# Kernel tuning notes

Hardware: AMD Instinct MI355X
Metric: run time of the kernel (lower is better)

Reference implementation:

```python
import jax, jax.numpy as jnp
import numpy as np
from jax import lax

HID = 256   # hidden_size
NN = 25     # n_nodes
T = 50      # seq_len
FIN = 16    # obs_length + 4
AS = 8      # action_space
HEADS = 5   # gat_head_num
E = 100     # edges per graph
B = 256     # batch


def setup_inputs() -> dict:
    key = jax.random.key(0)
    ks = jax.random.split(key, 32)
    s = 0.02
    def p(i, shape):
        return jax.random.normal(ks[i], shape, jnp.float32) * s
    return {
        "obs": jax.random.normal(ks[0], (B, NN, T, FIN), jnp.float32),
        "obs_map": jax.random.normal(ks[1], (B, 3, 84, 84), jnp.float32),
        "edges": jax.random.randint(ks[2], (B, 2, E), 0, NN),
        "edges_feature": jax.random.normal(ks[3], (B, E, 4), jnp.float32),
        "mlp_w": p(4, (FIN, HID)), "mlp_b": p(5, (HID,)),
        "c1_w": p(6, (32, 3, 8, 8)), "c1_b": p(7, (32,)),
        "c2_w": p(8, (64, 32, 4, 4)), "c2_b": p(9, (64,)),
        "c3_w": p(10, (64, 64, 3, 3)), "c3_b": p(11, (64,)),
        "fc_w": p(12, (3136, HID)), "fc_b": p(13, (HID,)),
        "gru_wih": p(14, (3 * HID, HID)), "gru_whh": p(15, (3 * HID, HID)),
        "gru_bih": p(16, (3 * HID,)), "gru_bhh": p(17, (3 * HID,)),
        "gat_wl": p(18, (HID, HEADS * HID)), "gat_bl": p(19, (HEADS * HID,)),
        "gat_wr": p(20, (HID, HEADS * HID)), "gat_br": p(21, (HEADS * HID,)),
        "gat_att": p(22, (HEADS, HID)), "gat_bias": p(23, (HID,)),
        "hid_w": p(24, (HID, HID)), "hid_b": p(25, (HID,)),
        "out_w": p(26, (HID, 1)), "out_b": p(27, (1,)),
        "adv_w": p(28, (HID, AS)), "adv_b": p(29, (AS,)),
    }


def _cnn(x, c1w, c1b, c2w, c2b, c3w, c3b, fcw, fcb):
    # Nature-CNN encoder: [B,3,84,84] -> [B,HID]
    dn = ('NCHW', 'OIHW', 'NCHW')
    h = jax.nn.relu(lax.conv_general_dilated(x, c1w, (4, 4), 'VALID', dimension_numbers=dn) + c1b[None, :, None, None])
    h = jax.nn.relu(lax.conv_general_dilated(h, c2w, (2, 2), 'VALID', dimension_numbers=dn) + c2b[None, :, None, None])
    h = jax.nn.relu(lax.conv_general_dilated(h, c3w, (1, 1), 'VALID', dimension_numbers=dn) + c3b[None, :, None, None])
    h = h.reshape(h.shape[0], -1)  # [B, 64*7*7]
    return jax.nn.relu(h @ fcw + fcb)


def _gru_last(x, wih, whh, bih, bhh):
    # torch nn.GRU (batch_first), return final hidden state [B,H]
    H = whh.shape[1]
    xg = x @ wih.T + bih  # precompute input gates [B,T,3H]
    def step(h, xg_t):
        hg = h @ whh.T + bhh
        xr, xz, xn = jnp.split(xg_t, 3, axis=-1)
        hr, hz, hn = jnp.split(hg, 3, axis=-1)
        r = jax.nn.sigmoid(xr + hr)
        z = jax.nn.sigmoid(xz + hz)
        n = jnp.tanh(xn + r * hn)
        return (1.0 - z) * n + z * h, None
    h0 = jnp.zeros((x.shape[0], H), x.dtype)
    hT, _ = lax.scan(step, h0, jnp.swapaxes(xg, 0, 1))
    return hT


def _gat(x, ei, wl, bl, wr, br, att, gbias):
    # GATv2Conv (concat=False): one graph, x [N,H], ei [2,E'] incl. self loops
    n = x.shape[0]
    heads, ch = att.shape
    src, dst = ei[0], ei[1]
    gl = (x @ wl + bl).reshape(n, heads, ch)
    gr = (x @ wr + br).reshape(n, heads, ch)
    e = jax.nn.leaky_relu(gl[src] + gr[dst], 0.2)          # [E',H,C]
    score = jnp.einsum('ehc,hc->eh', e, att)               # [E',H]
    m = jax.ops.segment_max(score, dst, num_segments=n)
    ex = jnp.exp(score - m[dst])
    den = jax.ops.segment_sum(ex, dst, num_segments=n)
    alpha = ex / den[dst]                                   # softmax per dst node
    out = jax.ops.segment_sum(alpha[:, :, None] * gl[src], dst, num_segments=n)
    return out.mean(axis=1) + gbias, alpha                  # mean over heads (concat=False)


def reference(obs, obs_map, edges, edges_feature, mlp_w, mlp_b, c1_w, c1_b, c2_w, c2_b, c3_w, c3_b, fc_w, fc_b, gru_wih, gru_whh, gru_bih, gru_bhh, gat_wl, gat_bl, gat_wr, gat_br, gat_att, gat_bias, hid_w, hid_b, out_w, out_b, adv_w, adv_b):
    bsz, n = obs.shape[0], obs.shape[1]
    n_edges = edges.shape[2]
    target_emb = _cnn(obs_map, c1_w, c1_b, c2_w, c2_b, c3_w, c3_b, fc_w, fc_b)[:, None, :]
    nbrs = obs[:, 1:].reshape(bsz * (n - 1), obs.shape[2], obs.shape[3])
    nbrs_emb = jax.nn.relu(nbrs @ mlp_w + mlp_b)            # MLP_rnn (Linear+ReLU)
    nbrs_h = _gru_last(nbrs_emb, gru_wih, gru_whh, gru_bih, gru_bhh).reshape(bsz, n - 1, -1)
    node_emb = jnp.concatenate([target_emb, nbrs_h], axis=1)  # [B,N,HID]
    loops = jnp.broadcast_to(jnp.arange(n)[None, None, :], (bsz, 2, n))
    ei = jnp.concatenate([edges, loops], axis=2)            # PyG add_self_loops (appended)
    gat_out, alpha = jax.vmap(lambda xg, eg: _gat(xg, eg, gat_wl, gat_bl, gat_wr, gat_br, gat_att, gat_bias))(node_emb, ei)
    att_w = alpha[:, : n_edges + 1].mean(axis=-1)           # matches att_weights[:-n_nodes+1].mean(axis=1)
    h = jax.nn.relu(gat_out[:, 0] @ hid_w + hid_b)          # only node-0 feature used
    v = h @ out_w + out_b
    adv = h @ adv_w + adv_b
    q = v + (adv - adv.mean(axis=-1, keepdims=True))        # dueling head
    return q, att_w
```

## Files before the change

### kernel.cpp

```cpp
#include <hip/hip_runtime.h>
#include <cstdint>

typedef __attribute__((ext_vector_type(8))) __bf16 bf16x8;
typedef __attribute__((ext_vector_type(4))) float f32x4;
typedef __attribute__((ext_vector_type(4))) unsigned int uint4v;
typedef __attribute__((ext_vector_type(2))) unsigned int uint2v;
typedef __attribute__((ext_vector_type(4))) float float4v;
typedef __attribute__((ext_vector_type(2))) long long2v;

__device__ __forceinline__ unsigned short f2bf(float x){
  union { float f; unsigned u; } v; v.f = x;
  unsigned r = v.u + 0x7FFFu + ((v.u >> 16) & 1u);
  return (unsigned short)(r >> 16);
}
__device__ __forceinline__ float bf2f(unsigned short h){
  union { unsigned u; float f; } v; v.u = ((unsigned)h) << 16;
  return v.f;
}
__device__ __forceinline__ float bflo(unsigned u){
  union { unsigned x; float f; } v; v.x = u << 16; return v.f;
}
__device__ __forceinline__ float bfhi(unsigned u){
  union { unsigned x; float f; } v; v.x = u & 0xFFFF0000u; return v.f;
}
__device__ __forceinline__ f32x4 MFMA16(bf16x8 a, bf16x8 b, f32x4 c){
  return __builtin_amdgcn_mfma_f32_16x16x32_bf16(a, b, c, 0, 0, 0);
}
__device__ __forceinline__ f32x4 MFMA8(long a, long b, f32x4 c){
  return __builtin_amdgcn_mfma_f32_16x16x32_fp8_fp8(a, b, c, 0, 0, 0);
}
__device__ __forceinline__ unsigned char f2fp8(float x){
  int p = __builtin_amdgcn_cvt_pk_fp8_f32(x, x, 0, false);
  return (unsigned char)(p & 0xFF);
}

__global__ __launch_bounds__(256) void prep_k(
    const float* __restrict__ wih, const float* __restrict__ whh,
    const float* __restrict__ wl, const float* __restrict__ wr,
    const float* __restrict__ bl, const float* __restrict__ br,
    const float* __restrict__ fcw, const float* __restrict__ mlpw,
    unsigned char* __restrict__ wfrag8, unsigned short* __restrict__ mlpfrag,
    unsigned short* __restrict__ wlrT, unsigned short* __restrict__ fcwT,
    float* __restrict__ blbr){
  int i = blockIdx.x*256 + threadIdx.x;
  if (i < 393216){
    int b16 = i & 15;
    int l   = (i >> 4) & 63;
    int chunk = i >> 10;
    int wkp = chunk / 6;
    int mg  = chunk - 6*wkp;
    int w = wkp >> 2, kkp = wkp & 3;
    int ks = b16 >> 3, e = b16 & 7;
    int kk = kkp*2 + ks;
    int mat = mg / 3, g = mg - 3*(mg/3);
    int n = g*256 + w*16 + (l & 15);
    int k = kk*32 + (l >> 4)*8 + e;
    float v = 16.f * (mat ? whh[n*256 + k] : wih[n*256 + k]);
    wfrag8[i] = f2fp8(v);
    return;
  }
  i -= 393216;
  if (i < 8192){
    int w = i >> 9;
    int r4 = i & 511;
    int l = r4 >> 3, e = r4 & 7;
    int n = w*16 + (l & 15);
    int k = (l >> 4)*8 + e;
    mlpfrag[i] = (k < 16) ? f2bf(mlpw[k*256 + n]) : (unsigned short)0;
    return;
  }
  i -= 8192;
  if (i < 655360){
    int n = i >> 8, k = i & 255;
    float v = (n < 1280) ? wl[k*1280 + n] : wr[k*1280 + (n-1280)];
    wlrT[i] = f2bf(v); return;
  }
  i -= 655360;
  if (i < 802816){
    int n = i / 3136, k = i - n*3136;
    fcwT[i] = f2bf(fcw[k*256 + n]); return;
  }
  i -= 802816;
  if (i < 2560){
    blbr[i] = (i < 1280) ? bl[i] : br[i-1280];
  }
}

__global__ __launch_bounds__(256) void conv2_k(const unsigned short* __restrict__ in,
              const float* __restrict__ w, const float* __restrict__ bias,
              unsigned short* __restrict__ out){
  __shared__ unsigned short in_s[32][20][20];
  __shared__ float w_s[16][32][4][4];
  __shared__ float b_s[16];
  int bid = blockIdx.x; int b = bid >> 2, h = bid & 3;
  int t = threadIdx.x;
  for (int idx = t; idx < 32*400; idx += 256) ((unsigned short*)in_s)[idx] = in[(size_t)b*12800 + idx];
  for (int idx = t; idx < 16*512; idx += 256) ((float*)w_s)[idx] = w[h*8192 + idx];
  if (t < 16) b_s[t] = bias[h*16 + t];
  __syncthreads();
  for (int p = t; p < 432; p += 256){
    int ocl = p / 27; int rem = p - ocl*27;
    int oy = rem / 3, og = rem - oy*3;
    float a0=b_s[ocl],a1=b_s[ocl],a2=b_s[ocl];
    #pragma unroll 4
    for (int ic=0;ic<32;ic++){
      #pragma unroll
      for (int ky=0;ky<4;ky++){
        const unsigned short* row = &in_s[ic][oy*2+ky][og*6];
        float s[8];
        #pragma unroll
        for (int cc=0;cc<8;cc++) s[cc]=bf2f(row[cc]);
        const float* wp = &w_s[ocl][ic][ky][0];
        #pragma unroll
        for (int kx=0;kx<4;kx++){
          float wv = wp[kx];
          a0 += s[kx]*wv; a1 += s[2+kx]*wv; a2 += s[4+kx]*wv;
        }
      }
    }
    size_t ob = ((size_t)(b*64 + h*16+ocl)*9 + oy)*9 + og*3;
    out[ob+0]=f2bf(fmaxf(a0,0.f)); out[ob+1]=f2bf(fmaxf(a1,0.f)); out[ob+2]=f2bf(fmaxf(a2,0.f));
  }
}

__global__ __launch_bounds__(256) void conv3_k(const unsigned short* __restrict__ in,
              const float* __restrict__ w, const float* __restrict__ bias,
              unsigned short* __restrict__ out){
  __shared__ unsigned short in_s[64][9][9];
  __shared__ float w_s[16][64][3][3];
  __shared__ float b_s[16];
  int bid = blockIdx.x; int b = bid >> 2, h = bid & 3;
  int t = threadIdx.x;
  for (int idx = t; idx < 64*81; idx += 256) ((unsigned short*)in_s)[idx] = in[(size_t)b*5184 + idx];
  for (int idx = t; idx < 16*576; idx += 256) ((float*)w_s)[idx] = w[h*9216 + idx];
  if (t < 16) b_s[t] = bias[h*16 + t];
  __syncthreads();
  for (int p = t; p < 224; p += 256){
    int ocl = p / 14; int rem = p - ocl*14;
    int oy = rem >> 1, og = rem & 1;
    int ox0 = og*4; int nx = og ? 3 : 4;
    float a[4]; a[0]=a[1]=a[2]=a[3]=b_s[ocl];
    for (int ic=0;ic<64;ic++){
      #pragma unroll
      for (int ky=0;ky<3;ky++){
        const unsigned short* row = &in_s[ic][oy+ky][ox0];
        float s[6];
        #pragma unroll
        for (int cc=0;cc<6;cc++) s[cc] = (ox0+cc < 9) ? bf2f(row[cc]) : 0.f;
        const float* wp = &w_s[ocl][ic][ky][0];
        #pragma unroll
        for (int kx=0;kx<3;kx++){
          float wv = wp[kx];
          #pragma unroll
          for (int jj=0;jj<4;jj++) a[jj] += s[jj+kx]*wv;
        }
      }
    }
    size_t ob = (size_t)b*3136 + (h*16+ocl)*49 + oy*7 + ox0;
    #pragma unroll
    for (int jj=0;jj<4;jj++) if (jj < nx) out[ob+jj] = f2bf(fmaxf(a[jj],0.f));
  }
}

__global__ __launch_bounds__(256) void gemm_k(const unsigned short* __restrict__ A,
              const unsigned short* __restrict__ B, const float* __restrict__ bias,
              unsigned short* __restrict__ C, int K, int ldc, int rowmul, int relu, int Nblk){
  __shared__ __align__(16) unsigned short As[64*32];
  __shared__ __align__(16) unsigned short Bs[64*32];
  int bid = blockIdx.x;
  int nb = bid % Nblk, mb = bid / Nblk;
  int t = threadIdx.x;
  int w = t >> 6, l = t & 63, lr = l & 15, lh = l >> 4;
  int sr = t >> 2, sq = t & 3;
  f32x4 acc[4];
  #pragma unroll
  for (int i=0;i<4;i++) acc[i] = (f32x4){0.f,0.f,0.f,0.f};
  int nkk = K >> 5;
  const size_t a_row = (size_t)(mb*64 + sr)*K;
  const size_t b_row = (size_t)(nb*64 + sr)*K;
  for (int kk=0;kk<nkk;kk++){
    uint4v av = *(const uint4v*)&A[a_row + kk*32 + sq*8];
    uint4v bv = *(const uint4v*)&B[b_row + kk*32 + sq*8];
    __syncthreads();
    *(uint4v*)((char*)As + ((sr*64 + sq*16) ^ ((sr&3)<<4))) = av;
    *(uint4v*)((char*)Bs + ((sr*64 + sq*16) ^ ((sr&3)<<4))) = bv;
    __syncthreads();
    int brow = w*16 + lr;
    bf16x8 bfr = *(const bf16x8*)((char*)Bs + ((brow*64 + lh*16) ^ ((brow&3)<<4)));
    #pragma unroll
    for (int mt=0;mt<4;mt++){
      int arow = mt*16 + lr;
      bf16x8 afr = *(const bf16x8*)((char*)As + ((arow*64 + lh*16) ^ ((arow&3)<<4)));
      acc[mt] = MFMA16(afr, bfr, acc[mt]);
    }
  }
  int col = nb*64 + w*16 + lr;
  float bn = bias[col];
  #pragma unroll
  for (int mt=0;mt<4;mt++){
    #pragma unroll
    for (int r=0;r<4;r++){
      int row = mb*64 + mt*16 + lh*4 + r;
      float v = acc[mt][r] + bn;
      if (relu) v = fmaxf(v, 0.f);
      C[(size_t)row*rowmul*ldc + col] = f2bf(v);
    }
  }
}

__global__ __launch_bounds__(256) void gemm_fc_k(const unsigned short* __restrict__ A,
              const unsigned short* __restrict__ B, float* __restrict__ P){
  __shared__ __align__(16) unsigned short As[64*32];
  __shared__ __align__(16) unsigned short Bs[64*32];
  int bid = blockIdx.x;
  int s = bid % 7, tile = bid / 7;
  int nb = tile & 3, mb = tile >> 2;
  int t = threadIdx.x;
  int w = t >> 6, l = t & 63, lr = l & 15, lh = l >> 4;
  int sr = t >> 2, sq = t & 3;
  f32x4 acc[4];
  #pragma unroll
  for (int i=0;i<4;i++) acc[i] = (f32x4){0.f,0.f,0.f,0.f};
  const int K = 3136;
  const size_t a_row = (size_t)(mb*64 + sr)*K;
  const size_t b_row = (size_t)(nb*64 + sr)*K;
  for (int kk = s*14; kk < s*14 + 14; kk++){
    uint4v av = *(const uint4v*)&A[a_row + kk*32 + sq*8];
    uint4v bv = *(const uint4v*)&B[b_row + kk*32 + sq*8];
    __syncthreads();
    *(uint4v*)((char*)As + ((sr*64 + sq*16) ^ ((sr&3)<<4))) = av;
    *(uint4v*)((char*)Bs + ((sr*64 + sq*16) ^ ((sr&3)<<4))) = bv;
    __syncthreads();
    int brow = w*16 + lr;
    bf16x8 bfr = *(const bf16x8*)((char*)Bs + ((brow*64 + lh*16) ^ ((brow&3)<<4)));
    #pragma unroll
    for (int mt=0;mt<4;mt++){
      int arow = mt*16 + lr;
      bf16x8 afr = *(const bf16x8*)((char*)As + ((arow*64 + lh*16) ^ ((arow&3)<<4)));
      acc[mt] = MFMA16(afr, bfr, acc[mt]);
    }
  }
  int col = nb*64 + w*16 + lr;
  #pragma unroll
  for (int mt=0;mt<4;mt++){
    #pragma unroll
    for (int r=0;r<4;r++){
      int row = mb*64 + mt*16 + lh*4 + r;
      P[(size_t)s*65536 + row*256 + col] = acc[mt][r];
    }
  }
}

__global__ __launch_bounds__(256) void fc_red_k(const float* __restrict__ P,
              const float* __restrict__ fcb, unsigned short* __restrict__ nemb){
  int idx = blockIdx.x*256 + threadIdx.x;
  int row = idx >> 8, col = idx & 255;
  float sum = fcb[col];
  #pragma unroll
  for (int k=0;k<7;k++) sum += P[k*65536 + idx];
  nemb[(size_t)row*25*256 + col] = f2bf(fmaxf(sum, 0.f));
}

__global__ __launch_bounds__(1024, 4)
void gruconv_k(const float* __restrict__ obs,
              const unsigned char* __restrict__ wfrag8,
              const unsigned short* __restrict__ mlpfrag,
              const float* __restrict__ mlpb,
              const float* __restrict__ bih, const float* __restrict__ bhh,
              unsigned short* __restrict__ nemb,
              const float* __restrict__ cin, const float* __restrict__ c1w,
              const float* __restrict__ c1b, unsigned short* __restrict__ c1o){
  __shared__ __align__(16) char smem[121984];

  const int t = threadIdx.x, blk = blockIdx.x;

  if (blk >= 192){
    float* in_s = (float*)smem;
    float* w_s  = (float*)(smem + 96768);
    float* b_s  = (float*)(smem + 121344);
    int b = blk - 192;
    int q = t >> 8, t2 = t & 255;
    float* inq = in_s + q*6048;
    for (int idx = t2; idx < 3*24*84; idx += 256){
      int ic = idx / (24*84); int rem = idx - ic*(24*84);
      int iy = rem / 84, ix = rem - iy*84;
      inq[idx] = cin[((size_t)(b*3+ic)*84 + (q*20 + iy))*84 + ix];
    }
    for (int idx = t; idx < 32*192; idx += 1024) w_s[idx] = c1w[idx];
    if (t < 32) b_s[t] = c1b[t];
    __syncthreads();
    for (int p = t2; p < 800; p += 256){
      int oc = p / 25; int rem = p - oc*25;
      int oy = rem / 5, og = rem - oy*5;
      float a0=b_s[oc],a1=b_s[oc],a2=b_s[oc],a3=b_s[oc];
      #pragma unroll
      for (int ic=0;ic<3;ic++){
        #pragma unroll
        for (int ky=0;ky<8;ky++){
          const float* row = &inq[(ic*24 + oy*4+ky)*84 + og*16];
          float s[20];
          #pragma unroll
          for (int cc=0;cc<20;cc++) s[cc]=row[cc];
          const float* wp = &w_s[(oc*3 + ic)*64 + ky*8];
          #pragma unroll
          for (int kx=0;kx<8;kx++){
            float wv = wp[kx];
            a0 += s[kx]*wv; a1 += s[4+kx]*wv; a2 += s[8+kx]*wv; a3 += s[12+kx]*wv;
          }
        }
      }
      size_t ob = ((size_t)(b*32+oc)*20 + (q*5+oy))*20 + og*4;
      c1o[ob+0]=f2bf(fmaxf(a0,0.f)); c1o[ob+1]=f2bf(fmaxf(a1,0.f));
      c1o[ob+2]=f2bf(fmaxf(a2,0.f)); c1o[ob+3]=f2bf(fmaxf(a3,0.f));
    }
    return;
  }

  unsigned short* obsA = (unsigned short*)smem;
  unsigned char* e8_0 = (unsigned char*)(smem + 2048);
  unsigned char* e8_1 = (unsigned char*)(smem + 10240);
  unsigned char* h8   = (unsigned char*)(smem + 18432);

  obsA[t & 1023] = 0;
  for (int j = t; j < 8192; j += 1024) h8[j] = 0;

  const int w = t >> 6, l = t & 63, lr = l & 15, lh = l >> 4;
  const int jcol = w*16 + lr;
  const float bR  = bih[jcol]     + bhh[jcol];
  const float bZ  = bih[256+jcol] + bhh[256+jcol];
  const float bXN = bih[512+jcol];
  const float bHN = bhh[512+jcol];
  const float bMb = mlpb[jcol];
  const bf16x8 bMLP = *(const bf16x8*)(mlpfrag + w*512 + l*8);

  const unsigned char* wb8 = wfrag8 + w*24576 + l*16;

  const int srow = t >> 2, sk4 = t & 3;
  int rrS = blk*32 + srow; int bS = rrS/24, ndS = 1 + (rrS - bS*24);
  const float* obase4 = obs + (size_t)(bS*25 + ndS)*800 + sk4*4;
  const int obyte = (srow*64 + sk4*8) ^ ((srow&3)<<4);

  const int a8off = lr*256 + lh*8;
  const int xr8 = lr << 3;
  const int o16 = lh*16;
  const int oa0b = (lr*64 + o16) ^ ((lr&3)<<4);
  const int oa1b = ((16+lr)*64 + o16) ^ ((lr&3)<<4);
  const int hw0 = jcol;
  const float S = 1.f/256.f;

  f32x4 hs0 = (f32x4){0.f,0.f,0.f,0.f};
  f32x4 hs1 = (f32x4){0.f,0.f,0.f,0.f};

#define EMB_COMPUTE(DST) { \
  f32x4 e0 = (f32x4){0.f,0.f,0.f,0.f}, e1 = (f32x4){0.f,0.f,0.f,0.f}; \
  bf16x8 oa0 = *(const bf16x8*)((char*)obsA + oa0b); \
  bf16x8 oa1 = *(const bf16x8*)((char*)obsA + oa1b); \
  e0 = MFMA16(oa0, bMLP, e0); \
  e1 = MFMA16(oa1, bMLP, e1); \
  _Pragma("unroll") \
  for (int r=0;r<4;r++){ \
    int m = lh*4 + r; \
    (DST)[(m*256 + hw0) ^ ((m&15)<<3)] = f2fp8(fmaxf(e0[r] + bMb, 0.f)*16.f); \
    int m2 = m + 16; \
    (DST)[(m2*256 + hw0) ^ ((m2&15)<<3)] = f2fp8(fmaxf(e1[r] + bMb, 0.f)*16.f); \
  } }

  __syncthreads();
  if (t < 128){
    float4v ov = *(const float4v*)(obase4);
    uint2v pk;
    pk[0] = (unsigned)f2bf(ov[0]) | ((unsigned)f2bf(ov[1]) << 16);
    pk[1] = (unsigned)f2bf(ov[2]) | ((unsigned)f2bf(ov[3]) << 16);
    *(uint2v*)((char*)obsA + obyte) = pk;
  }
  __syncthreads();
  EMB_COMPUTE(e8_0)
  __syncthreads();

  for (int step=0; step<50; step++){
    const unsigned char* ebuf = (step & 1) ? e8_1 : e8_0;
    unsigned char* nbuf = (step & 1) ? e8_0 : e8_1;
    const bool stg = (t < 128) && (step < 49);
    float4v ov;
    if (stg) ov = *(const float4v*)(obase4 + (size_t)(step+1)*16);

    f32x4 aR0=(f32x4){0,0,0,0}, aR1=(f32x4){0,0,0,0};
    f32x4 aZ0=(f32x4){0,0,0,0}, aZ1=(f32x4){0,0,0,0};
    f32x4 aN0=(f32x4){0,0,0,0}, aN1=(f32x4){0,0,0,0};
    f32x4 aM0=(f32x4){0,0,0,0}, aM1=(f32x4){0,0,0,0};
    __builtin_amdgcn_s_setprio(1);
    #pragma unroll 2
    for (int kkp=0;kkp<4;kkp++){
      const unsigned char* wk8 = wb8 + kkp*6144;
      long2v wIR = *(const long2v*)(wk8);
      long2v wIZ = *(const long2v*)(wk8 + 1024);
      long2v wIN = *(const long2v*)(wk8 + 2048);
      long2v wHR = *(const long2v*)(wk8 + 3072);
      long2v wHZ = *(const long2v*)(wk8 + 4096);
      long2v wHN = *(const long2v*)(wk8 + 5120);
      {
        int kk = kkp*2;
        int ab = a8off + kk*32;
        long eA0 = *(const long*)(ebuf + (ab ^ xr8));
        long eA1 = *(const long*)(ebuf + ((ab + 4096) ^ xr8));
        long hA0 = *(const long*)(h8 + (ab ^ xr8));
        long hA1 = *(const long*)(h8 + ((ab + 4096) ^ xr8));
        aR0 = MFMA8(eA0, wIR[0], aR0);  aR0 = MFMA8(hA0, wHR[0], aR0);
        aR1 = MFMA8(eA1, wIR[0], aR1);  aR1 = MFMA8(hA1, wHR[0], aR1);
        aZ0 = MFMA8(eA0, wIZ[0], aZ0);  aZ0 = MFMA8(hA0, wHZ[0], aZ0);
        aZ1 = MFMA8(eA1, wIZ[0], aZ1);  aZ1 = MFMA8(hA1, wHZ[0], aZ1);
        aN0 = MFMA8(eA0, wIN[0], aN0);  aN1 = MFMA8(eA1, wIN[0], aN1);
        aM0 = MFMA8(hA0, wHN[0], aM0);  aM1 = MFMA8(hA1, wHN[0], aM1);
      }
      {
        int kk = kkp*2 + 1;
        int ab = a8off + kk*32;
        long eA0 = *(const long*)(ebuf + (ab ^ xr8));
        long eA1 = *(const long*)(ebuf + ((ab + 4096) ^ xr8));
        long hA0 = *(const long*)(h8 + (ab ^ xr8));
        long hA1 = *(const long*)(h8 + ((ab + 4096) ^ xr8));
        aR0 = MFMA8(eA0, wIR[1], aR0);  aR0 = MFMA8(hA0, wHR[1], aR0);
        aR1 = MFMA8(eA1, wIR[1], aR1);  aR1 = MFMA8(hA1, wHR[1], aR1);
        aZ0 = MFMA8(eA0, wIZ[1], aZ0);  aZ0 = MFMA8(hA0, wHZ[1], aZ0);
        aZ1 = MFMA8(eA1, wIZ[1], aZ1);  aZ1 = MFMA8(hA1, wHZ[1], aZ1);
        aN0 = MFMA8(eA0, wIN[1], aN0);  aN1 = MFMA8(eA1, wIN[1], aN1);
        aM0 = MFMA8(hA0, wHN[1], aM0);  aM1 = MFMA8(hA1, wHN[1], aM1);
      }
    }
    __builtin_amdgcn_s_setprio(0);
    if (stg){
      uint2v pk;
      pk[0] = (unsigned)f2bf(ov[0]) | ((unsigned)f2bf(ov[1]) << 16);
      pk[1] = (unsigned)f2bf(ov[2]) | ((unsigned)f2bf(ov[3]) << 16);
      *(uint2v*)((char*)obsA + obyte) = pk;
    }
    __syncthreads();
    if (step < 49){
      EMB_COMPUTE(nbuf)
    }
    #pragma unroll
    for (int mt=0;mt<2;mt++){
      f32x4 vR = mt ? aR1 : aR0;
      f32x4 vZ = mt ? aZ1 : aZ0;
      f32x4 vN = mt ? aN1 : aN0;
      f32x4 vM = mt ? aM1 : aM0;
      #pragma unroll
      for (int r=0;r<4;r++){
        float rp = vR[r]*S + bR;
        float zp = vZ[r]*S + bZ;
        float xn = vN[r]*S + bXN;
        float hn = vM[r]*S + bHN;
        float rg = 1.f/(1.f + __expf(-rp));
        float zg = 1.f/(1.f + __expf(-zp));
        float arg = xn + rg*hn;
        float e2 = __expf(2.f*arg);
        float nv = (e2 - 1.f)/(e2 + 1.f);
        float hold = mt ? hs1[r] : hs0[r];
        float hnew = (1.f - zg)*nv + zg*hold;
        if (mt) hs1[r] = hnew; else hs0[r] = hnew;
        int m = mt*16 + lh*4 + r;
        h8[(m*256 + hw0) ^ ((m&15)<<3)] = f2fp8(hnew*16.f);
        if (step == 49){
          int rr = blk*32 + m; int b = rr/24; int nd = 1 + (rr - b*24);
          nemb[(size_t)(b*25+nd)*256 + jcol] = f2bf(hnew);
        }
      }
    }
    __syncthreads();
  }
#undef EMB_COMPUTE
}

__global__ __launch_bounds__(256) void gat_k(const int* __restrict__ edges,
              const unsigned short* __restrict__ glgr,
              const float* __restrict__ att, const float* __restrict__ gbias,
              const float* __restrict__ hidw, const float* __restrict__ hidb,
              const float* __restrict__ outw, const float* __restrict__ outb,
              const float* __restrict__ advw, const float* __restrict__ advb,
              float* __restrict__ out){
  __shared__ int src_s[125], dst_s[125];
  __shared__ __align__(16) float att_s[1280];
  __shared__ float sc[125][5], al[125][5];
  __shared__ float mx[25][5], dn[25][5];
  __shared__ float g0[256], hh[256];
  __shared__ float adv_s[8], v_s;
  __shared__ int e0[125]; __shared__ int ne0;

  int b = blockIdx.x, t = threadIdx.x;
  if (t < 100){ src_s[t] = edges[b*200 + t]; dst_s[t] = edges[b*200 + 100 + t]; }
  else if (t < 125){ src_s[t] = t - 100; dst_s[t] = t - 100; }
  for (int j = t; j < 1280; j += 256) att_s[j] = att[j];
  __syncthreads();
  if (t == 0){ int c = 0; for (int e=0;e<125;e++) if (dst_s[e]==0) e0[c++]=e; ne0 = c; }
  const unsigned short* gbase = glgr + (size_t)b*25*2560;
  for (int p = t; p < 625; p += 256){
    int e = p/5, h = p - 5*(p/5);
    const unsigned short* glp = gbase + src_s[e]*2560 + h*256;
    const unsigned short* grp = gbase + dst_s[e]*2560 + 1280 + h*256;
    const float* ap = &att_s[h*256];
    float acc = 0.f;
    #pragma unroll 4
    for (int c=0;c<256;c+=8){
      uint4v gu = *(const uint4v*)&glp[c];
      uint4v ru = *(const uint4v*)&grp[c];
      #pragma unroll
      for (int q=0;q<4;q++){
        float s0 = bflo(gu[q]) + bflo(ru[q]);
        float s1 = bfhi(gu[q]) + bfhi(ru[q]);
        s0 = (s0 > 0.f) ? s0 : 0.2f*s0;
        s1 = (s1 > 0.f) ? s1 : 0.2f*s1;
        acc += s0*ap[c+2*q] + s1*ap[c+2*q+1];
      }
    }
    sc[e][h] = acc;
  }
  __syncthreads();
  if (t < 125){
    int j = t/5, h = t - 5*(t/5);
    float m = -1e30f;
    for (int e=0;e<125;e++) if (dst_s[e]==j) m = fmaxf(m, sc[e][h]);
    float d = 0.f;
    for (int e=0;e<125;e++) if (dst_s[e]==j) d += __expf(sc[e][h]-m);
    mx[j][h] = m; dn[j][h] = d;
  }
  __syncthreads();
  for (int p = t; p < 625; p += 256){
    int e = p/5, h = p - 5*(p/5);
    int dd = dst_s[e];
    al[e][h] = __expf(sc[e][h] - mx[dd][h]) / dn[dd][h];
  }
  __syncthreads();
  if (t < 101){
    out[2048 + b*101 + t] = (al[t][0]+al[t][1]+al[t][2]+al[t][3]+al[t][4])*0.2f;
  }
  {
    float acc = 0.f;
    for (int x=0;x<ne0;x++){
      int e = e0[x]; int s = src_s[e];
      const unsigned short* glp = gbase + s*2560 + t;
      #pragma unroll
      for (int h=0;h<5;h++) acc += al[e][h]*bf2f(glp[h*256]);
    }
    g0[t] = acc*0.2f + gbias[t];
  }
  __syncthreads();
  {
    float acc = hidb[t];
    for (int k=0;k<256;k++) acc += g0[k]*hidw[k*256+t];
    hh[t] = fmaxf(acc, 0.f);
  }
  __syncthreads();
  if (t < 8){
    float acc = advb[t];
    for (int k=0;k<256;k++) acc += hh[k]*advw[k*8+t];
    adv_s[t] = acc;
  } else if (t == 8){
    float acc = outb[0];
    for (int k=0;k<256;k++) acc += hh[k]*outw[k];
    v_s = acc;
  }
  __syncthreads();
  if (t < 8){
    float m = adv_s[0]+adv_s[1]+adv_s[2]+adv_s[3]+adv_s[4]+adv_s[5]+adv_s[6]+adv_s[7];
    out[b*8+t] = v_s + adv_s[t] - m*0.125f;
  }
}

extern "C" void kernel_launch(void* const* d_in, const int* in_sizes, int n_in,
                              void* d_out, int out_size, void* d_ws, size_t ws_size,
                              hipStream_t stream){
  const float* obs     = (const float*)d_in[0];
  const float* obs_map = (const float*)d_in[1];
  const int*   edges   = (const int*)d_in[2];
  const float* mlp_w = (const float*)d_in[4];
  const float* mlp_b = (const float*)d_in[5];
  const float* c1w = (const float*)d_in[6];  const float* c1b = (const float*)d_in[7];
  const float* c2w = (const float*)d_in[8];  const float* c2b = (const float*)d_in[9];
  const float* c3w = (const float*)d_in[10]; const float* c3b = (const float*)d_in[11];
  const float* fcw = (const float*)d_in[12]; const float* fcb = (const float*)d_in[13];
  const float* wih = (const float*)d_in[14]; const float* whh = (const float*)d_in[15];
  const float* bih = (const float*)d_in[16]; const float* bhh = (const float*)d_in[17];
  const float* gwl = (const float*)d_in[18]; const float* gbl = (const float*)d_in[19];
  const float* gwr = (const float*)d_in[20]; const float* gbr = (const float*)d_in[21];
  const float* gatt = (const float*)d_in[22]; const float* gbias = (const float*)d_in[23];
  const float* hidw = (const float*)d_in[24]; const float* hidb = (const float*)d_in[25];
  const float* outw = (const float*)d_in[26]; const float* outb = (const float*)d_in[27];
  const float* advw = (const float*)d_in[28]; const float* advb = (const float*)d_in[29];
  float* out = (float*)d_out;
  char* ws = (char*)d_ws;

  unsigned short* c1o  = (unsigned short*)(ws + 0);
  unsigned short* c2o  = (unsigned short*)(ws + 6553600);
  unsigned short* c3o  = (unsigned short*)(ws + 9207808);
  float*          fcpart = (float*)(ws + 16000000);
  unsigned short* glgr = (unsigned short*)(ws + 0);
  size_t o = 32768000;
  unsigned short* nemb    = (unsigned short*)(ws + o); o += 3276800;
  unsigned char*  wfrag8  = (unsigned char*)(ws + o);  o += 393216;
  unsigned short* mlpfrag = (unsigned short*)(ws + o); o += 16384;
  unsigned short* wlrT    = (unsigned short*)(ws + o); o += 1310720;
  unsigned short* fcwT    = (unsigned short*)(ws + o); o += 1605632;
  float* blbr             = (float*)(ws + o); o += 10240;

  prep_k<<<7274, 256, 0, stream>>>(wih, whh, gwl, gwr, gbl, gbr, fcw, mlp_w, wfrag8, mlpfrag, wlrT, fcwT, blbr);
  gruconv_k<<<448, 1024, 0, stream>>>(obs, wfrag8, mlpfrag, mlp_b, bih, bhh, nemb,
                                      obs_map, c1w, c1b, c1o);
  conv2_k<<<1024, 256, 0, stream>>>(c1o, c2w, c2b, c2o);
  conv3_k<<<1024, 256, 0, stream>>>(c2o, c3w, c3b, c3o);
  gemm_fc_k<<<112, 256, 0, stream>>>(c3o, fcwT, fcpart);
  fc_red_k<<<256, 256, 0, stream>>>(fcpart, fcb, nemb);
  gemm_k<<<4000, 256, 0, stream>>>(nemb, wlrT, blbr, glgr, 256, 2560, 1, 0, 40);
  gat_k<<<256, 256, 0, stream>>>(edges, glgr, gatt, gbias, hidw, hidb, outw, outb, advw, advb, out);
}
```

Before: 728.8 us.

## Fuse conv2 and conv3 into the CNN branch of the GRU kernel

Runs conv1, conv2 and conv3 for each image inside the CNN blocks of the combined GRU/conv kernel and keeps intermediate activations in shared memory instead of writing them to global memory. The separate conv2/conv3 launches are removed. Conv weights are pre-converted to bf16 in the prep kernel. CNN blocks drop from 256 to 64, each looping over 4 images, with simpler one-output-per-thread inner loops. This removes the global round trips and two launches, but it cuts CNN parallelism, reloads the conv2/conv3 weights for every image, and raises shared memory per block.

```diff
diff --git a/kernel.cpp b/kernel.cpp
--- a/kernel.cpp
+++ b/kernel.cpp
@@ -39,9 +39,11 @@
     const float* __restrict__ wl, const float* __restrict__ wr,
     const float* __restrict__ bl, const float* __restrict__ br,
     const float* __restrict__ fcw, const float* __restrict__ mlpw,
+    const float* __restrict__ c2w, const float* __restrict__ c3w,
     unsigned char* __restrict__ wfrag8, unsigned short* __restrict__ mlpfrag,
     unsigned short* __restrict__ wlrT, unsigned short* __restrict__ fcwT,
-    float* __restrict__ blbr){
+    float* __restrict__ blbr,
+    unsigned short* __restrict__ c2wb, unsigned short* __restrict__ c3wb){
   int i = blockIdx.x*256 + threadIdx.x;
   if (i < 393216){
     int b16 = i & 15;
@@ -83,83 +85,12 @@
   i -= 802816;
   if (i < 2560){
     blbr[i] = (i < 1280) ? bl[i] : br[i-1280];
-  }
-}
-
-__global__ __launch_bounds__(256) void conv2_k(const unsigned short* __restrict__ in,
-              const float* __restrict__ w, const float* __restrict__ bias,
-              unsigned short* __restrict__ out){
-  __shared__ unsigned short in_s[32][20][20];
-  __shared__ float w_s[16][32][4][4];
-  __shared__ float b_s[16];
-  int bid = blockIdx.x; int b = bid >> 2, h = bid & 3;
-  int t = threadIdx.x;
-  for (int idx = t; idx < 32*400; idx += 256) ((unsigned short*)in_s)[idx] = in[(size_t)b*12800 + idx];
-  for (int idx = t; idx < 16*512; idx += 256) ((float*)w_s)[idx] = w[h*8192 + idx];
-  if (t < 16) b_s[t] = bias[h*16 + t];
-  __syncthreads();
-  for (int p = t; p < 432; p += 256){
-    int ocl = p / 27; int rem = p - ocl*27;
-    int oy = rem / 3, og = rem - oy*3;
-    float a0=b_s[ocl],a1=b_s[ocl],a2=b_s[ocl];
-    #pragma unroll 4
-    for (int ic=0;ic<32;ic++){
-      #pragma unroll
-      for (int ky=0;ky<4;ky++){
-        const unsigned short* row = &in_s[ic][oy*2+ky][og*6];
-        float s[8];
-        #pragma unroll
-        for (int cc=0;cc<8;cc++) s[cc]=bf2f(row[cc]);
-        const float* wp = &w_s[ocl][ic][ky][0];
-        #pragma unroll
-        for (int kx=0;kx<4;kx++){
-          float wv = wp[kx];
-          a0 += s[kx]*wv; a1 += s[2+kx]*wv; a2 += s[4+kx]*wv;
-        }
-      }
-    }
-    size_t ob = ((size_t)(b*64 + h*16+ocl)*9 + oy)*9 + og*3;
-    out[ob+0]=f2bf(fmaxf(a0,0.f)); out[ob+1]=f2bf(fmaxf(a1,0.f)); out[ob+2]=f2bf(fmaxf(a2,0.f));
-  }
-}
-
-__global__ __launch_bounds__(256) void conv3_k(const unsigned short* __restrict__ in,
-              const float* __restrict__ w, const float* __restrict__ bias,
-              unsigned short* __restrict__ out){
-  __shared__ unsigned short in_s[64][9][9];
-  __shared__ float w_s[16][64][3][3];
-  __shared__ float b_s[16];
-  int bid = blockIdx.x; int b = bid >> 2, h = bid & 3;
-  int t = threadIdx.x;
-  for (int idx = t; idx < 64*81; idx += 256) ((unsigned short*)in_s)[idx] = in[(size_t)b*5184 + idx];
-  for (int idx = t; idx < 16*576; idx += 256) ((float*)w_s)[idx] = w[h*9216 + idx];
-  if (t < 16) b_s[t] = bias[h*16 + t];
-  __syncthreads();
-  for (int p = t; p < 224; p += 256){
-    int ocl = p / 14; int rem = p - ocl*14;
-    int oy = rem >> 1, og = rem & 1;
-    int ox0 = og*4; int nx = og ? 3 : 4;
-    float a[4]; a[0]=a[1]=a[2]=a[3]=b_s[ocl];
-    for (int ic=0;ic<64;ic++){
-      #pragma unroll
-      for (int ky=0;ky<3;ky++){
-        const unsigned short* row = &in_s[ic][oy+ky][ox0];
-        float s[6];
-        #pragma unroll
-        for (int cc=0;cc<6;cc++) s[cc] = (ox0+cc < 9) ? bf2f(row[cc]) : 0.f;
-        const float* wp = &w_s[ocl][ic][ky][0];
-        #pragma unroll
-        for (int kx=0;kx<3;kx++){
-          float wv = wp[kx];
-          #pragma unroll
-          for (int jj=0;jj<4;jj++) a[jj] += s[jj+kx]*wv;
-        }
-      }
-    }
-    size_t ob = (size_t)b*3136 + (h*16+ocl)*49 + oy*7 + ox0;
-    #pragma unroll
-    for (int jj=0;jj<4;jj++) if (jj < nx) out[ob+jj] = f2bf(fmaxf(a[jj],0.f));
-  }
+    return;
+  }
+  i -= 2560;
+  if (i < 32768){ c2wb[i] = f2bf(c2w[i]); return; }
+  i -= 32768;
+  if (i < 36864){ c3wb[i] = f2bf(c3w[i]); }
 }
 
 __global__ __launch_bounds__(256) void gemm_k(const unsigned short* __restrict__ A,
@@ -269,49 +200,87 @@
               const float* __restrict__ bih, const float* __restrict__ bhh,
               unsigned short* __restrict__ nemb,
               const float* __restrict__ cin, const float* __restrict__ c1w,
-              const float* __restrict__ c1b, unsigned short* __restrict__ c1o){
-  __shared__ __align__(16) char smem[121984];
+              const float* __restrict__ c1b,
+              const unsigned short* __restrict__ c2wb, const float* __restrict__ c2b,
+              const unsigned short* __restrict__ c3wb, const float* __restrict__ c3b,
+              unsigned short* __restrict__ c3o){
+  __shared__ __align__(16) char smem[135040];
 
   const int t = threadIdx.x, blk = blockIdx.x;
 
   if (blk >= 192){
-    float* in_s = (float*)smem;
-    float* w_s  = (float*)(smem + 96768);
-    float* b_s  = (float*)(smem + 121344);
-    int b = blk - 192;
-    int q = t >> 8, t2 = t & 255;
-    float* inq = in_s + q*6048;
-    for (int idx = t2; idx < 3*24*84; idx += 256){
-      int ic = idx / (24*84); int rem = idx - ic*(24*84);
-      int iy = rem / 84, ix = rem - iy*84;
-      inq[idx] = cin[((size_t)(b*3+ic)*84 + (q*20 + iy))*84 + ix];
-    }
-    for (int idx = t; idx < 32*192; idx += 1024) w_s[idx] = c1w[idx];
-    if (t < 32) b_s[t] = c1b[t];
-    __syncthreads();
-    for (int p = t2; p < 800; p += 256){
-      int oc = p / 25; int rem = p - oc*25;
-      int oy = rem / 5, og = rem - oy*5;
-      float a0=b_s[oc],a1=b_s[oc],a2=b_s[oc],a3=b_s[oc];
-      #pragma unroll
-      for (int ic=0;ic<3;ic++){
+    float* img = (float*)smem;
+    float* w1  = (float*)(smem + 84672);
+    float* b1  = (float*)(smem + 109248);
+    unsigned short* c1s = (unsigned short*)(smem + 109376);
+    unsigned short* w2s = (unsigned short*)smem;
+    float* b2  = (float*)(smem + 65536);
+    unsigned short* c2s = (unsigned short*)(smem + 76160);
+    unsigned short* w3s = (unsigned short*)smem;
+    float* b3  = (float*)(smem + 73728);
+    int cb = blk - 192;
+    for (int idx = t; idx < 6144; idx += 1024) w1[idx] = c1w[idx];
+    if (t < 32) b1[t] = c1b[t];
+    for (int i=0;i<4;i++){
+      int b = cb + (i<<6);
+      __syncthreads();
+      for (int idx = t; idx < 21168; idx += 1024) img[idx] = cin[(size_t)b*21168 + idx];
+      __syncthreads();
+      for (int p = t; p < 12800; p += 1024){
+        int oc = p / 400; int rem = p - oc*400;
+        int oy = rem / 20, ox = rem - (rem/20)*20;
+        float a = b1[oc];
         #pragma unroll
-        for (int ky=0;ky<8;ky++){
-          const float* row = &inq[(ic*24 + oy*4+ky)*84 + og*16];
-          float s[20];
+        for (int ic=0;ic<3;ic++){
           #pragma unroll
-          for (int cc=0;cc<20;cc++) s[cc]=row[cc];
-          const float* wp = &w_s[(oc*3 + ic)*64 + ky*8];
-          #pragma unroll
-          for (int kx=0;kx<8;kx++){
-            float wv = wp[kx];
-            a0 += s[kx]*wv; a1 += s[4+kx]*wv; a2 += s[8+kx]*wv; a3 += s[12+kx]*wv;
+          for (int ky=0;ky<8;ky++){
+            const float* row = &img[(ic*84 + oy*4+ky)*84 + ox*4];
+            const float* wp = &w1[(oc*3 + ic)*64 + ky*8];
+            #pragma unroll
+            for (int kx=0;kx<8;kx++) a += row[kx]*wp[kx];
           }
         }
-      }
-      size_t ob = ((size_t)(b*32+oc)*20 + (q*5+oy))*20 + og*4;
-      c1o[ob+0]=f2bf(fmaxf(a0,0.f)); c1o[ob+1]=f2bf(fmaxf(a1,0.f));
-      c1o[ob+2]=f2bf(fmaxf(a2,0.f)); c1o[ob+3]=f2bf(fmaxf(a3,0.f));
+        c1s[p] = f2bf(fmaxf(a, 0.f));
+      }
+      __syncthreads();
+      for (int idx = t; idx < 32768; idx += 1024) w2s[idx] = c2wb[idx];
+      if (t < 64) b2[t] = c2b[t];
+      __syncthreads();
+      for (int p = t; p < 5184; p += 1024){
+        int oc = p / 81; int rem = p - oc*81;
+        int oy = rem / 9, ox = rem - (rem/9)*9;
+        float a = b2[oc];
+        #pragma unroll 4
+        for (int ic=0;ic<32;ic++){
+          #pragma unroll
+          for (int ky=0;ky<4;ky++){
+            const unsigned short* row = &c1s[(ic*20 + oy*2+ky)*20 + ox*2];
+            const unsigned short* wp = &w2s[((oc*32+ic)*4+ky)*4];
+            #pragma unroll
+            for (int kx=0;kx<4;kx++) a += bf2f(row[kx])*bf2f(wp[kx]);
+          }
+        }
+        c2s[p] = f2bf(fmaxf(a, 0.f));
+      }
+      __syncthreads();
+      for (int idx = t; idx < 36864; idx += 1024) w3s[idx] = c3wb[idx];
+      if (t < 64) b3[t] = c3b[t];
+      __syncthreads();
+      for (int p = t; p < 3136; p += 1024){
+        int oc = p / 49; int rem = p - oc*49;
+        int oy = rem / 7, ox = rem - (rem/7)*7;
+        float a = b3[oc];
+        for (int ic=0;ic<64;ic++){
+          #pragma unroll
+          for (int ky=0;ky<3;ky++){
+            const unsigned short* row = &c2s[(ic*9 + oy+ky)*9 + ox];
+            const unsigned short* wp = &w3s[((oc*64+ic)*3+ky)*3];
+            #pragma unroll
+            for (int kx=0;kx<3;kx++) a += bf2f(row[kx])*bf2f(wp[kx]);
+          }
+        }
+        c3o[(size_t)b*3136 + p] = f2bf(fmaxf(a, 0.f));
+      }
     }
     return;
   }
@@ -589,9 +558,7 @@
   float* out = (float*)d_out;
   char* ws = (char*)d_ws;
 
-  unsigned short* c1o  = (unsigned short*)(ws + 0);
-  unsigned short* c2o  = (unsigned short*)(ws + 6553600);
-  unsigned short* c3o  = (unsigned short*)(ws + 9207808);
+  unsigned short* c3o  = (unsigned short*)(ws + 0);
   float*          fcpart = (float*)(ws + 16000000);
   unsigned short* glgr = (unsigned short*)(ws + 0);
   size_t o = 32768000;
@@ -601,12 +568,13 @@
   unsigned short* wlrT    = (unsigned short*)(ws + o); o += 1310720;
   unsigned short* fcwT    = (unsigned short*)(ws + o); o += 1605632;
   float* blbr             = (float*)(ws + o); o += 10240;
-
-  prep_k<<<7274, 256, 0, stream>>>(wih, whh, gwl, gwr, gbl, gbr, fcw, mlp_w, wfrag8, mlpfrag, wlrT, fcwT, blbr);
-  gruconv_k<<<448, 1024, 0, stream>>>(obs, wfrag8, mlpfrag, mlp_b, bih, bhh, nemb,
-                                      obs_map, c1w, c1b, c1o);
-  conv2_k<<<1024, 256, 0, stream>>>(c1o, c2w, c2b, c2o);
-  conv3_k<<<1024, 256, 0, stream>>>(c2o, c3w, c3b, c3o);
+  unsigned short* c2wb    = (unsigned short*)(ws + o); o += 65536;
+  unsigned short* c3wb    = (unsigned short*)(ws + o); o += 73728;
+
+  prep_k<<<7546, 256, 0, stream>>>(wih, whh, gwl, gwr, gbl, gbr, fcw, mlp_w, c2w, c3w,
+                                   wfrag8, mlpfrag, wlrT, fcwT, blbr, c2wb, c3wb);
+  gruconv_k<<<256, 1024, 0, stream>>>(obs, wfrag8, mlpfrag, mlp_b, bih, bhh, nemb,
+                                      obs_map, c1w, c1b, c2wb, c2b, c3wb, c3b, c3o);
   gemm_fc_k<<<112, 256, 0, stream>>>(c3o, fcwT, fcpart);
   fc_red_k<<<256, 256, 0, stream>>>(fcpart, fcb, nemb);
   gemm_k<<<4000, 256, 0, stream>>>(nemb, wlrT, blbr, glgr, 256, 2560, 1, 0, 40);
```

Result: slower. 2.320 ms (+218.3%).
